# Optimization experiments

Hardware: AMD Instinct MI355X
Metric: run time of the kernel (lower is better)

The kernel has to match this reference:

```python
import jax, jax.numpy as jnp
import numpy as np

B, CI, HW, K, C, NH, L = 512, 3, 28, 28 // 28 and 0 or 7, 1024, 16, 12
K = 7


def setup_inputs() -> dict:
    key = jax.random.key(0)
    ks = jax.random.split(key, 8)
    s = 0.02
    return {
        "x": jax.random.normal(ks[0], (B, CI, HW, HW), jnp.float32),
        "conv_w": jax.random.normal(ks[1], (C, CI, K, K), jnp.float32) * s,  # Conv2d weight [Co,Ci,k,k], shared with deconv
        "ln1_w": jnp.ones((L, C), jnp.float32),
        "ln1_b": jnp.zeros((L, C), jnp.float32),
        "wq": jax.random.normal(ks[2], (L, C, C), jnp.float32) * s,
        "wk": jax.random.normal(ks[3], (L, C, C), jnp.float32) * s,
        "wv": jax.random.normal(ks[4], (L, C, C), jnp.float32) * s,
        "ln2_w": jnp.ones((L, C), jnp.float32),
        "ln2_b": jnp.zeros((L, C), jnp.float32),
        "mlp_w": jax.random.normal(ks[5], (L, C, C), jnp.float32) * s,
        "mlp_b": jnp.zeros((L, C), jnp.float32),
        "out_w": jax.random.normal(ks[6], (C, C), jnp.float32) * s,
        "out_b": jnp.zeros((C,), jnp.float32),
        "head_num": NH,
    }


def _layernorm(x, w, b, eps=1e-5):
    m = jnp.mean(x, axis=-1, keepdims=True)
    v = jnp.var(x, axis=-1, keepdims=True)  # biased var, matches torch LayerNorm
    return (x - m) * jax.lax.rsqrt(v + eps) * w + b


def _attn(h, wq, wk, wv, nh):
    b, t, c = h.shape
    hd = c // nh
    q = (h @ wq.T).reshape(b, t, nh, hd).transpose(0, 2, 1, 3)  # [B,H,T,hd]
    k = (h @ wk.T).reshape(b, t, nh, hd).transpose(0, 2, 1, 3)
    v = (h @ wv.T).reshape(b, t, nh, hd).transpose(0, 2, 1, 3)
    scores = jnp.einsum("bhqd,bhkd->bhqk", q, k) / jnp.sqrt(jnp.float32(hd))
    mask = jnp.tril(jnp.ones((t, t), bool))
    scores = jnp.where(mask, scores, -jnp.inf)
    a = jax.nn.softmax(scores, axis=-1)
    o = jnp.einsum("bhqk,bhkd->bhqd", a, v)
    return o.transpose(0, 2, 1, 3).reshape(b, t, c)


def _forward(x, conv_w, ln1_w, ln1_b, wq, wk, wv, ln2_w, ln2_b, mlp_w, mlp_b, out_w, out_b, head_num):
    b, ci, hh, ww = x.shape
    co, _, k, _ = conv_w.shape
    # thumbnail: bilinear downsample to (k,k) (align_corners=False == half-pixel), then k-strided conv -> [B,Co]
    thumb = jax.image.resize(x, (b, ci, k, k), method="bilinear", antialias=False)
    thumb_tok = jnp.einsum("bcpq,dcpq->bd", thumb, conv_w)
    # kernel==stride conv == patchify + matmul
    hp, wp = hh // k, ww // k
    xp = x.reshape(b, ci, hp, k, wp, k)
    patches = jnp.einsum("bcipjq,dcpq->bdij", xp, conv_w).reshape(b, co, hp * wp)
    h = jnp.concatenate([thumb_tok[:, :, None], patches], axis=-1).transpose(0, 2, 1)  # [B,T=1+hp*wp,C]
    nlayers = ln1_w.shape[0]
    for l in range(nlayers):
        a = _attn(_layernorm(h, ln1_w[l], ln1_b[l]), wq[l], wk[l], wv[l], head_num)
        h = h + a
        m = _layernorm(h, ln2_w[l], ln2_b[l]) @ mlp_w[l].T + mlp_b[l]
        h = h + m
    logits = h @ out_w.T + out_b  # [B,T,C]
    # decode: ConvTranspose2d(kernel=stride=k) with shared weight; input [B,Co,1,T] -> [B,Ci,k,T*k]
    z = logits.transpose(0, 2, 1)  # [B,Co,T]
    t = z.shape[-1]
    out = jnp.einsum("bcs,cdhw->bdhsw", z, conv_w).reshape(b, ci, k, t * k)
    return out


def reference(x, conv_w, ln1_w, ln1_b, wq, wk, wv, ln2_w, ln2_b, mlp_w, mlp_b, out_w, out_b, head_num):
    return _forward(x, conv_w, ln1_w, ln1_b, wq, wk, wv, ln2_w, ln2_b, mlp_w, mlp_b, out_w, out_b, head_num)
```

## Files before the change

### kernel.cpp

```cpp
#include <hip/hip_runtime.h>


typedef unsigned short u16;
typedef short bfrag8 __attribute__((ext_vector_type(8)));
typedef float facc4 __attribute__((ext_vector_type(4)));

__device__ __forceinline__ u16 f2bf(float f) {
  union { float f; unsigned u; } x; x.f = f;
  unsigned r = x.u + 0x7fffu + ((x.u >> 16) & 1u);
  return (u16)(r >> 16);
}
__device__ __forceinline__ float bf2f(u16 h) {
  union { unsigned u; float f; } x; x.u = ((unsigned)h) << 16;
  return x.f;
}

template <int MODE>
__global__ __launch_bounds__(256) void gemm_bt(
    const u16* __restrict__ A, int lda,
    const u16* __restrict__ B0, const u16* __restrict__ B1, const u16* __restrict__ B2,
    int ldb, int K,
    void* __restrict__ outp, long long zstride, int ldo,
    const float* __restrict__ bias)
{
  __shared__ __align__(16) u16 As[128 * 32];
  __shared__ __align__(16) u16 Bs[128 * 32];

  const int m0 = blockIdx.x * 128;
  const int n0 = blockIdx.y * 128;
  const int z  = blockIdx.z;
  const u16* __restrict__ B = (z == 0) ? B0 : ((z == 1) ? B1 : B2);

  const int tid  = threadIdx.x;
  const int wave = tid >> 6;
  const int lane = tid & 63;
  const int wm   = (wave >> 1) * 64;
  const int wn   = (wave & 1) * 64;
  const int lrow = lane & 15;
  const int lquad = lane >> 4;

  facc4 acc[4][4] = {};

  const int c0 = tid;        const int r0 = c0 >> 2; const int k0c = (c0 & 3) << 3;
  const int c1 = tid + 256;  const int r1 = c1 >> 2; const int k1c = (c1 & 3) << 3;

  for (int k0 = 0; k0 < K; k0 += 32) {
    const u16* ga0 = A + (long long)(m0 + r0) * lda + (k0 + k0c);
    const u16* ga1 = A + (long long)(m0 + r1) * lda + (k0 + k1c);
    const u16* gb0 = B + (long long)(n0 + r0) * ldb + (k0 + k0c);
    const u16* gb1 = B + (long long)(n0 + r1) * ldb + (k0 + k1c);
    __builtin_amdgcn_global_load_lds((const __attribute__((address_space(1))) void*)ga0,
                                     (__attribute__((address_space(3))) void*)(As + c0 * 8), 16, 0, 0);
    __builtin_amdgcn_global_load_lds((const __attribute__((address_space(1))) void*)ga1,
                                     (__attribute__((address_space(3))) void*)(As + c1 * 8), 16, 0, 0);
    __builtin_amdgcn_global_load_lds((const __attribute__((address_space(1))) void*)gb0,
                                     (__attribute__((address_space(3))) void*)(Bs + c0 * 8), 16, 0, 0);
    __builtin_amdgcn_global_load_lds((const __attribute__((address_space(1))) void*)gb1,
                                     (__attribute__((address_space(3))) void*)(Bs + c1 * 8), 16, 0, 0);
    __syncthreads();

    bfrag8 af[4], bfr[4];
#pragma unroll
    for (int im = 0; im < 4; ++im)
      af[im] = *(const bfrag8*)(As + (wm + im * 16 + lrow) * 32 + lquad * 8);
#pragma unroll
    for (int in = 0; in < 4; ++in)
      bfr[in] = *(const bfrag8*)(Bs + (wn + in * 16 + lrow) * 32 + lquad * 8);
#pragma unroll
    for (int im = 0; im < 4; ++im)
#pragma unroll
      for (int in = 0; in < 4; ++in)
        acc[im][in] = __builtin_amdgcn_mfma_f32_16x16x32_bf16(af[im], bfr[in], acc[im][in], 0, 0, 0);
    __syncthreads();
  }

#pragma unroll
  for (int in = 0; in < 4; ++in) {
    const int col = n0 + wn + in * 16 + lrow;
    const float bb = bias ? bias[col] : 0.0f;
#pragma unroll
    for (int im = 0; im < 4; ++im) {
#pragma unroll
      for (int r = 0; r < 4; ++r) {
        const int row = m0 + wm + im * 16 + lquad * 4 + r;
        const long long off = (long long)row * ldo + col;
        const float v = acc[im][in][r] + bb;
        if (MODE == 0)       ((float*)outp)[off] = v;
        else if (MODE == 1)  (((u16*)outp) + zstride * z)[off] = f2bf(v);
        else                 ((float*)outp)[off] += v;
      }
    }
  }
}

__global__ __launch_bounds__(256) void ln_kernel(
    const float* __restrict__ h, const float* __restrict__ w,
    const float* __restrict__ b, u16* __restrict__ out)
{
  const long long row = blockIdx.x;
  const float* __restrict__ x = h + row * 1024;
  const int t = threadIdx.x;
  float v0 = x[t], v1 = x[t + 256], v2 = x[t + 512], v3 = x[t + 768];
  float s = v0 + v1 + v2 + v3;
  float q = v0 * v0 + v1 * v1 + v2 * v2 + v3 * v3;
  for (int o = 32; o > 0; o >>= 1) { s += __shfl_down(s, o); q += __shfl_down(q, o); }
  __shared__ float ss[4], sq[4];
  const int wave = t >> 6, lane = t & 63;
  if (lane == 0) { ss[wave] = s; sq[wave] = q; }
  __syncthreads();
  const float st = ss[0] + ss[1] + ss[2] + ss[3];
  const float qt = sq[0] + sq[1] + sq[2] + sq[3];
  const float mean = st * (1.0f / 1024.0f);
  const float var = qt * (1.0f / 1024.0f) - mean * mean;
  const float inv = rsqrtf(var + 1e-5f);
  u16* o2 = out + row * 1024;
  o2[t]       = f2bf((v0 - mean) * inv * w[t]       + b[t]);
  o2[t + 256] = f2bf((v1 - mean) * inv * w[t + 256] + b[t + 256]);
  o2[t + 512] = f2bf((v2 - mean) * inv * w[t + 512] + b[t + 512]);
  o2[t + 768] = f2bf((v3 - mean) * inv * w[t + 768] + b[t + 768]);
}

__global__ __launch_bounds__(256) void attn_kernel(const u16* __restrict__ QKV,
                                                   float* __restrict__ h)
{
  const int blk = blockIdx.x;
  const int b = blk >> 4, head = blk & 15;
  __shared__ float qs[17][64], ks[17][64], vs[17][64];
  __shared__ float sc[17][20];
  const long long base = (long long)b * 17 * 1024 + head * 64;
  const u16* Q  = QKV;
  const u16* Kp = QKV + 8912896LL;
  const u16* V  = QKV + 17825792LL;

  for (int i = threadIdx.x; i < 17 * 64; i += 256) {
    const int t = i >> 6, d = i & 63;
    const long long off = base + (long long)t * 1024 + d;
    qs[t][d] = bf2f(Q[off]); ks[t][d] = bf2f(Kp[off]); vs[t][d] = bf2f(V[off]);
  }
  __syncthreads();

  for (int i = threadIdx.x; i < 289; i += 256) {
    const int tq = i / 17, tk = i % 17;
    float a = 0.0f;
    if (tk <= tq) {
#pragma unroll
      for (int d = 0; d < 64; ++d) a += qs[tq][d] * ks[tk][d];
      a *= 0.125f;
    }
    sc[tq][tk] = a;
  }
  __syncthreads();

  if (threadIdx.x < 17) {
    const int tq = threadIdx.x;
    float m = -1e30f;
    for (int tk = 0; tk <= tq; ++tk) m = fmaxf(m, sc[tq][tk]);
    float s = 0.0f;
    for (int tk = 0; tk <= tq; ++tk) { const float e = __expf(sc[tq][tk] - m); sc[tq][tk] = e; s += e; }
    const float inv = 1.0f / s;
    for (int tk = 0; tk <= tq; ++tk) sc[tq][tk] *= inv;
  }
  __syncthreads();

  for (int i = threadIdx.x; i < 17 * 64; i += 256) {
    const int tq = i >> 6, d = i & 63;
    float a = 0.0f;
    for (int tk = 0; tk <= tq; ++tk) a += sc[tq][tk] * vs[tk][d];
    h[base + (long long)tq * 1024 + d] += a;
  }
}

__global__ void build_p(const float* __restrict__ x, u16* __restrict__ P)
{
  const int n = blockIdx.x;
  const int j = threadIdx.x;
  if (j >= 160) return;
  const int b = n / 17, t = n % 17;
  float val = 0.0f;
  if (j < 147) {
    const int c = j / 49, rem = j % 49, p = rem / 7, q = rem % 7;
    const float* xb = x + (long long)(b * 3 + c) * 784;
    if (t == 0) {
      const int r = 4 * p + 1, cc = 4 * q + 1;
      val = 0.25f * (xb[r * 28 + cc] + xb[r * 28 + cc + 1] +
                     xb[(r + 1) * 28 + cc] + xb[(r + 1) * 28 + cc + 1]);
    } else {
      const int s = t - 1, ii = s >> 2, jj = s & 3;
      val = xb[(7 * ii + p) * 28 + 7 * jj + q];
    }
  }
  P[(long long)n * 160 + j] = f2bf(val);
}

__global__ __launch_bounds__(256) void cvt_conv(const float* __restrict__ cw,
                                                u16* __restrict__ Wc, u16* __restrict__ cw2)
{
  const int i = blockIdx.x * 256 + threadIdx.x;
  if (i < 163840) {
    const int d = i / 160, j = i % 160;
    Wc[i] = (j < 147) ? f2bf(cw[d * 147 + j]) : (u16)0;
  } else {
    const int i2 = i - 163840;
    if (i2 < 262144) {
      const int j = i2 / 1024, c = i2 % 1024;
      cw2[i2] = (j < 147) ? f2bf(cw[c * 147 + j]) : (u16)0;
    }
  }
}

__global__ __launch_bounds__(256) void cvt4(const float* __restrict__ a0, const float* __restrict__ a1,
                                            const float* __restrict__ a2, const float* __restrict__ a3,
                                            u16* __restrict__ o3, u16* __restrict__ om)
{
  const int i = blockIdx.x * 256 + threadIdx.x;
  const int which = i >> 20, off = i & 1048575;
  const float* src = (which == 0) ? a0 : (which == 1) ? a1 : (which == 2) ? a2 : a3;
  const float v = src[off];
  if (which < 3) o3[which * 1048576 + off] = f2bf(v);
  else           om[off] = f2bf(v);
}

__global__ __launch_bounds__(256) void cvtN(const float* __restrict__ in, u16* __restrict__ out, int n)
{
  const int i = blockIdx.x * 256 + threadIdx.x;
  if (i < n) out[i] = f2bf(in[i]);
}

__global__ __launch_bounds__(256) void scatter_out(const float* __restrict__ temp, float* __restrict__ out)
{
  const int i = blockIdx.x * 256 + threadIdx.x;
  if (i >= 1279488) return;
  const int wk = i % 7;
  const int r  = i / 7;
  const int s  = r % 17;
  const int r2 = r / 17;
  const int hk = r2 % 7;
  const int r3 = r2 / 7;
  const int d  = r3 % 3;
  const int b  = r3 / 3;
  out[i] = temp[(long long)(b * 17 + s) * 256 + d * 49 + hk * 7 + wk];
}

extern "C" void kernel_launch(void* const* d_in, const int* in_sizes, int n_in,
                              void* d_out, int out_size, void* d_ws, size_t ws_size,
                              hipStream_t stream)
{
  const float* x     = (const float*)d_in[0];
  const float* convw = (const float*)d_in[1];
  const float* ln1w  = (const float*)d_in[2];
  const float* ln1b  = (const float*)d_in[3];
  const float* wq    = (const float*)d_in[4];
  const float* wk    = (const float*)d_in[5];
  const float* wv    = (const float*)d_in[6];
  const float* ln2w  = (const float*)d_in[7];
  const float* ln2b  = (const float*)d_in[8];
  const float* mlpw  = (const float*)d_in[9];
  const float* mlpb  = (const float*)d_in[10];
  const float* outw  = (const float*)d_in[11];
  const float* outb  = (const float*)d_in[12];

  char* w = (char*)d_ws;
  float* h    = (float*)(w);
  u16*  Abuf  = (u16*)(w + 35651584);
  u16*  QKV   = (u16*)(w + 53477376);
  u16*  wb3   = (u16*)(w + 106954752);
  u16*  wmb   = (u16*)(w + 113246208);
  u16*  Wc    = (u16*)(w + 115343360);
  u16*  cw2   = (u16*)(w + 115671040);
  u16*  P     = (u16*)(w + 116195328);
  if (ws_size < 118980608ULL) return;

  cvt_conv<<<1664, 256, 0, stream>>>(convw, Wc, cw2);
  build_p<<<8704, 192, 0, stream>>>(x, P);
  gemm_bt<0><<<dim3(68, 8, 1), 256, 0, stream>>>(P, 160, Wc, Wc, Wc, 160, 160,
                                                 (void*)h, 0LL, 1024, nullptr);
  for (int l = 0; l < 12; ++l) {
    const size_t wo = (size_t)l * 1048576;
    cvt4<<<16384, 256, 0, stream>>>(wq + wo, wk + wo, wv + wo, mlpw + wo, wb3, wmb);
    ln_kernel<<<8704, 256, 0, stream>>>(h, ln1w + l * 1024, ln1b + l * 1024, Abuf);
    gemm_bt<1><<<dim3(68, 8, 3), 256, 0, stream>>>(Abuf, 1024, wb3, wb3 + 1048576, wb3 + 2097152,
                                                   1024, 1024, (void*)QKV, 8912896LL, 1024, nullptr);
    attn_kernel<<<8192, 256, 0, stream>>>(QKV, h);
    ln_kernel<<<8704, 256, 0, stream>>>(h, ln2w + l * 1024, ln2b + l * 1024, Abuf);
    gemm_bt<2><<<dim3(68, 8, 1), 256, 0, stream>>>(Abuf, 1024, wmb, wmb, wmb,
                                                   1024, 1024, (void*)h, 0LL, 1024, mlpb + l * 1024);
  }
  cvtN<<<34816, 256, 0, stream>>>(h, Abuf, 8912896);
  cvtN<<<4096, 256, 0, stream>>>(outw, wmb, 1048576);
  gemm_bt<1><<<dim3(68, 8, 1), 256, 0, stream>>>(Abuf, 1024, wmb, wmb, wmb,
                                                 1024, 1024, (void*)QKV, 0LL, 1024, outb);
  gemm_bt<0><<<dim3(68, 2, 1), 256, 0, stream>>>(QKV, 1024, cw2, cw2, cw2,
                                                 1024, 1024, (void*)h, 0LL, 256, nullptr);
  scatter_out<<<4998, 256, 0, stream>>>(h, (float*)d_out);
}
```

Before: 3.036 ms.

## Swizzle GEMM LDS layout, coalesce bf16 stores, batch weight conversion, fuse output scatter

Several changes at once. The GEMM's LDS tile now uses an XOR-swizzled layout with hoisted, precomputed addresses to cut bank conflicts. The bf16-output mode stages results through shared memory so global writes are 16-byte coalesced. A new cvt_all kernel converts all layer weights in one launch when the workspace is large, replacing twelve per-layer cvt4 launches. The final scatter_out kernel is dropped, and its index remapping moves into a new GEMM epilogue mode that writes directly to the output. The trade-off is added epilogue syncs and a larger workspace requirement for the batched-conversion path.

```diff
diff --git a/kernel.cpp b/kernel.cpp
--- a/kernel.cpp
+++ b/kernel.cpp
@@ -23,8 +23,9 @@
     void* __restrict__ outp, long long zstride, int ldo,
     const float* __restrict__ bias)
 {
-  __shared__ __align__(16) u16 As[128 * 32];
-  __shared__ __align__(16) u16 Bs[128 * 32];
+  __shared__ __align__(16) u16 smem[8192];
+  u16* const As = smem;
+  u16* const Bs = smem + 4096;
 
   const int m0 = blockIdx.x * 128;
   const int n0 = blockIdx.y * 128;
@@ -41,31 +42,39 @@
 
   facc4 acc[4][4] = {};
 
-  const int c0 = tid;        const int r0 = c0 >> 2; const int k0c = (c0 & 3) << 3;
-  const int c1 = tid + 256;  const int r1 = c1 >> 2; const int k1c = (c1 & 3) << 3;
+  int rA0, g0; { const int rp = tid >> 3, q = tid & 7, qp = q ^ (rp & 3);
+                 rA0 = rp * 2 + (qp >> 2); g0 = qp & 3; }
+  int rA1, g1; { const int s1 = tid + 256, rp = s1 >> 3, q = s1 & 7, qp = q ^ (rp & 3);
+                 rA1 = rp * 2 + (qp >> 2); g1 = qp & 3; }
+  const u16* ga0 = A + (long long)(m0 + rA0) * lda + g0 * 8;
+  const u16* ga1 = A + (long long)(m0 + rA1) * lda + g1 * 8;
+  const u16* gb0 = B + (long long)(n0 + rA0) * ldb + g0 * 8;
+  const u16* gb1 = B + (long long)(n0 + rA1) * ldb + g1 * 8;
+
+  const int ra = wm + lrow;
+  const int pa = (((ra & 1) << 2) | lquad) ^ ((ra >> 1) & 3);
+  const u16* const abase = As + (((ra >> 1) * 8 + pa) << 3);
+  const int rb = wn + lrow;
+  const int pb = (((rb & 1) << 2) | lquad) ^ ((rb >> 1) & 3);
+  const u16* const bbase = Bs + (((rb >> 1) * 8 + pb) << 3);
 
   for (int k0 = 0; k0 < K; k0 += 32) {
-    const u16* ga0 = A + (long long)(m0 + r0) * lda + (k0 + k0c);
-    const u16* ga1 = A + (long long)(m0 + r1) * lda + (k0 + k1c);
-    const u16* gb0 = B + (long long)(n0 + r0) * ldb + (k0 + k0c);
-    const u16* gb1 = B + (long long)(n0 + r1) * ldb + (k0 + k1c);
     __builtin_amdgcn_global_load_lds((const __attribute__((address_space(1))) void*)ga0,
-                                     (__attribute__((address_space(3))) void*)(As + c0 * 8), 16, 0, 0);
+                                     (__attribute__((address_space(3))) void*)(As + tid * 8), 16, 0, 0);
     __builtin_amdgcn_global_load_lds((const __attribute__((address_space(1))) void*)ga1,
-                                     (__attribute__((address_space(3))) void*)(As + c1 * 8), 16, 0, 0);
+                                     (__attribute__((address_space(3))) void*)(As + (tid + 256) * 8), 16, 0, 0);
     __builtin_amdgcn_global_load_lds((const __attribute__((address_space(1))) void*)gb0,
-                                     (__attribute__((address_space(3))) void*)(Bs + c0 * 8), 16, 0, 0);
+                                     (__attribute__((address_space(3))) void*)(Bs + tid * 8), 16, 0, 0);
     __builtin_amdgcn_global_load_lds((const __attribute__((address_space(1))) void*)gb1,
-                                     (__attribute__((address_space(3))) void*)(Bs + c1 * 8), 16, 0, 0);
+                                     (__attribute__((address_space(3))) void*)(Bs + (tid + 256) * 8), 16, 0, 0);
+    ga0 += 32; ga1 += 32; gb0 += 32; gb1 += 32;
     __syncthreads();
 
     bfrag8 af[4], bfr[4];
 #pragma unroll
-    for (int im = 0; im < 4; ++im)
-      af[im] = *(const bfrag8*)(As + (wm + im * 16 + lrow) * 32 + lquad * 8);
-#pragma unroll
-    for (int in = 0; in < 4; ++in)
-      bfr[in] = *(const bfrag8*)(Bs + (wn + in * 16 + lrow) * 32 + lquad * 8);
+    for (int im = 0; im < 4; ++im) af[im] = *(const bfrag8*)(abase + 512 * im);
+#pragma unroll
+    for (int in = 0; in < 4; ++in) bfr[in] = *(const bfrag8*)(bbase + 512 * in);
 #pragma unroll
     for (int im = 0; im < 4; ++im)
 #pragma unroll
@@ -74,20 +83,58 @@
     __syncthreads();
   }
 
+  if (MODE == 1) {
+    u16* const outb = ((u16*)outp) + zstride * z;
+    u16* const Ts = smem;
+#pragma unroll
+    for (int half = 0; half < 2; ++half) {
+      if ((wave >> 1) == half) {
+#pragma unroll
+        for (int in = 0; in < 4; ++in) {
+          const int col = wn + in * 16 + lrow;
+          const float bb = bias ? bias[n0 + col] : 0.0f;
+#pragma unroll
+          for (int im = 0; im < 4; ++im)
+#pragma unroll
+            for (int r = 0; r < 4; ++r)
+              Ts[(im * 16 + lquad * 4 + r) * 128 + col] = f2bf(acc[im][in][r] + bb);
+        }
+      }
+      __syncthreads();
+#pragma unroll
+      for (int it = 0; it < 4; ++it) {
+        const int g = it * 256 + tid;
+        const int row = g >> 4, colg = g & 15;
+        *(uint4*)(outb + (long long)(m0 + half * 64 + row) * ldo + n0 + colg * 8) =
+            *(const uint4*)(Ts + row * 128 + colg * 8);
+      }
+      __syncthreads();
+    }
+    return;
+  }
+
 #pragma unroll
   for (int in = 0; in < 4; ++in) {
     const int col = n0 + wn + in * 16 + lrow;
-    const float bb = bias ? bias[col] : 0.0f;
+    const float bb = (MODE != 3 && bias) ? bias[col] : 0.0f;
 #pragma unroll
     for (int im = 0; im < 4; ++im) {
 #pragma unroll
       for (int r = 0; r < 4; ++r) {
         const int row = m0 + wm + im * 16 + lquad * 4 + r;
-        const long long off = (long long)row * ldo + col;
         const float v = acc[im][in][r] + bb;
-        if (MODE == 0)       ((float*)outp)[off] = v;
-        else if (MODE == 1)  (((u16*)outp) + zstride * z)[off] = f2bf(v);
-        else                 ((float*)outp)[off] += v;
+        if (MODE == 0) {
+          ((float*)outp)[(long long)row * ldo + col] = v;
+        } else if (MODE == 2) {
+          ((float*)outp)[(long long)row * ldo + col] += v;
+        } else {
+          if (col < 147) {
+            const int b = row / 17, s = row - b * 17;
+            const int d = col / 49, rem = col - d * 49;
+            const int hk = rem / 7, wk = rem - hk * 7;
+            ((float*)outp)[(long long)((b * 3 + d) * 7 + hk) * 119 + s * 7 + wk] = v;
+          }
+        }
       }
     }
   }
@@ -208,6 +255,27 @@
   }
 }
 
+__global__ __launch_bounds__(256) void cvt_all(
+    const float* __restrict__ wq, const float* __restrict__ wk,
+    const float* __restrict__ wv, const float* __restrict__ mlpw,
+    const float* __restrict__ outw, u16* __restrict__ wAll)
+{
+  const int i = blockIdx.x * 256 + threadIdx.x;
+  const int which = i >> 18;
+  const int off = i & 262143;
+  const float4* src;
+  if (which < 48) {
+    const int layer = which >> 2, sub = which & 3;
+    const float* base = (sub == 0) ? wq : (sub == 1) ? wk : (sub == 2) ? wv : mlpw;
+    src = (const float4*)(base + (size_t)layer * 1048576) + off;
+  } else {
+    src = (const float4*)outw + off;
+  }
+  const float4 v = *src;
+  ushort4 o; o.x = f2bf(v.x); o.y = f2bf(v.y); o.z = f2bf(v.z); o.w = f2bf(v.w);
+  *(ushort4*)(wAll + (size_t)which * 1048576 + (size_t)off * 4) = o;
+}
+
 __global__ __launch_bounds__(256) void cvt4(const float* __restrict__ a0, const float* __restrict__ a1,
                                             const float* __restrict__ a2, const float* __restrict__ a3,
                                             u16* __restrict__ o3, u16* __restrict__ om)
@@ -224,21 +292,6 @@
 {
   const int i = blockIdx.x * 256 + threadIdx.x;
   if (i < n) out[i] = f2bf(in[i]);
-}
-
-__global__ __launch_bounds__(256) void scatter_out(const float* __restrict__ temp, float* __restrict__ out)
-{
-  const int i = blockIdx.x * 256 + threadIdx.x;
-  if (i >= 1279488) return;
-  const int wk = i % 7;
-  const int r  = i / 7;
-  const int s  = r % 17;
-  const int r2 = r / 17;
-  const int hk = r2 % 7;
-  const int r3 = r2 / 7;
-  const int d  = r3 % 3;
-  const int b  = r3 / 3;
-  out[i] = temp[(long long)(b * 17 + s) * 256 + d * 49 + hk * 7 + wk];
 }
 
 extern "C" void kernel_launch(void* const* d_in, const int* in_sizes, int n_in,
@@ -260,36 +313,69 @@
   const float* outb  = (const float*)d_in[12];
 
   char* w = (char*)d_ws;
-  float* h    = (float*)(w);
-  u16*  Abuf  = (u16*)(w + 35651584);
-  u16*  QKV   = (u16*)(w + 53477376);
-  u16*  wb3   = (u16*)(w + 106954752);
-  u16*  wmb   = (u16*)(w + 113246208);
-  u16*  Wc    = (u16*)(w + 115343360);
-  u16*  cw2   = (u16*)(w + 115671040);
-  u16*  P     = (u16*)(w + 116195328);
-  if (ws_size < 118980608ULL) return;
-
-  cvt_conv<<<1664, 256, 0, stream>>>(convw, Wc, cw2);
-  build_p<<<8704, 192, 0, stream>>>(x, P);
-  gemm_bt<0><<<dim3(68, 8, 1), 256, 0, stream>>>(P, 160, Wc, Wc, Wc, 160, 160,
-                                                 (void*)h, 0LL, 1024, nullptr);
-  for (int l = 0; l < 12; ++l) {
-    const size_t wo = (size_t)l * 1048576;
-    cvt4<<<16384, 256, 0, stream>>>(wq + wo, wk + wo, wv + wo, mlpw + wo, wb3, wmb);
-    ln_kernel<<<8704, 256, 0, stream>>>(h, ln1w + l * 1024, ln1b + l * 1024, Abuf);
-    gemm_bt<1><<<dim3(68, 8, 3), 256, 0, stream>>>(Abuf, 1024, wb3, wb3 + 1048576, wb3 + 2097152,
-                                                   1024, 1024, (void*)QKV, 8912896LL, 1024, nullptr);
-    attn_kernel<<<8192, 256, 0, stream>>>(QKV, h);
-    ln_kernel<<<8704, 256, 0, stream>>>(h, ln2w + l * 1024, ln2b + l * 1024, Abuf);
-    gemm_bt<2><<<dim3(68, 8, 1), 256, 0, stream>>>(Abuf, 1024, wmb, wmb, wmb,
-                                                   1024, 1024, (void*)h, 0LL, 1024, mlpb + l * 1024);
-  }
-  cvtN<<<34816, 256, 0, stream>>>(h, Abuf, 8912896);
-  cvtN<<<4096, 256, 0, stream>>>(outw, wmb, 1048576);
-  gemm_bt<1><<<dim3(68, 8, 1), 256, 0, stream>>>(Abuf, 1024, wmb, wmb, wmb,
-                                                 1024, 1024, (void*)QKV, 0LL, 1024, outb);
-  gemm_bt<0><<<dim3(68, 2, 1), 256, 0, stream>>>(QKV, 1024, cw2, cw2, cw2,
-                                                 1024, 1024, (void*)h, 0LL, 256, nullptr);
-  scatter_out<<<4998, 256, 0, stream>>>(h, (float*)d_out);
-}
+  const bool big = (ws_size >= 213352448ULL);
+
+  if (big) {
+    float* h   = (float*)(w);
+    u16* Abuf  = (u16*)(w + 35651584);
+    u16* QKV   = (u16*)(w + 53477376);
+    u16* wAll  = (u16*)(w + 106954752);
+    u16* Wc    = (u16*)(w + 209715200);
+    u16* cw2   = (u16*)(w + 210042880);
+    u16* P     = (u16*)(w + 210567168);
+
+    cvt_all<<<50176, 256, 0, stream>>>(wq, wk, wv, mlpw, outw, wAll);
+    cvt_conv<<<1664, 256, 0, stream>>>(convw, Wc, cw2);
+    build_p<<<8704, 192, 0, stream>>>(x, P);
+    gemm_bt<0><<<dim3(68, 8, 1), 256, 0, stream>>>(P, 160, Wc, Wc, Wc, 160, 160,
+                                                   (void*)h, 0LL, 1024, nullptr);
+    for (int l = 0; l < 12; ++l) {
+      u16* wl = wAll + (size_t)l * 4194304;
+      ln_kernel<<<8704, 256, 0, stream>>>(h, ln1w + l * 1024, ln1b + l * 1024, Abuf);
+      gemm_bt<1><<<dim3(68, 8, 3), 256, 0, stream>>>(Abuf, 1024, wl, wl + 1048576, wl + 2097152,
+                                                     1024, 1024, (void*)QKV, 8912896LL, 1024, nullptr);
+      attn_kernel<<<8192, 256, 0, stream>>>(QKV, h);
+      ln_kernel<<<8704, 256, 0, stream>>>(h, ln2w + l * 1024, ln2b + l * 1024, Abuf);
+      gemm_bt<2><<<dim3(68, 8, 1), 256, 0, stream>>>(Abuf, 1024, wl + 3145728, wl, wl,
+                                                     1024, 1024, (void*)h, 0LL, 1024, mlpb + l * 1024);
+    }
+    u16* wout = wAll + (size_t)48 * 1048576;
+    cvtN<<<34816, 256, 0, stream>>>(h, Abuf, 8912896);
+    gemm_bt<1><<<dim3(68, 8, 1), 256, 0, stream>>>(Abuf, 1024, wout, wout, wout,
+                                                   1024, 1024, (void*)QKV, 0LL, 1024, outb);
+    gemm_bt<3><<<dim3(68, 2, 1), 256, 0, stream>>>(QKV, 1024, cw2, cw2, cw2,
+                                                   1024, 1024, d_out, 0LL, 0, nullptr);
+  } else {
+    if (ws_size < 118980608ULL) return;
+    float* h   = (float*)(w);
+    u16* Abuf  = (u16*)(w + 35651584);
+    u16* QKV   = (u16*)(w + 53477376);
+    u16* wb3   = (u16*)(w + 106954752);
+    u16* wmb   = (u16*)(w + 113246208);
+    u16* Wc    = (u16*)(w + 115343360);
+    u16* cw2   = (u16*)(w + 115671040);
+    u16* P     = (u16*)(w + 116195328);
+
+    cvt_conv<<<1664, 256, 0, stream>>>(convw, Wc, cw2);
+    build_p<<<8704, 192, 0, stream>>>(x, P);
+    gemm_bt<0><<<dim3(68, 8, 1), 256, 0, stream>>>(P, 160, Wc, Wc, Wc, 160, 160,
+                                                   (void*)h, 0LL, 1024, nullptr);
+    for (int l = 0; l < 12; ++l) {
+      const size_t wo = (size_t)l * 1048576;
+      cvt4<<<16384, 256, 0, stream>>>(wq + wo, wk + wo, wv + wo, mlpw + wo, wb3, wmb);
+      ln_kernel<<<8704, 256, 0, stream>>>(h, ln1w + l * 1024, ln1b + l * 1024, Abuf);
+      gemm_bt<1><<<dim3(68, 8, 3), 256, 0, stream>>>(Abuf, 1024, wb3, wb3 + 1048576, wb3 + 2097152,
+                                                     1024, 1024, (void*)QKV, 8912896LL, 1024, nullptr);
+      attn_kernel<<<8192, 256, 0, stream>>>(QKV, h);
+      ln_kernel<<<8704, 256, 0, stream>>>(h, ln2w + l * 1024, ln2b + l * 1024, Abuf);
+      gemm_bt<2><<<dim3(68, 8, 1), 256, 0, stream>>>(Abuf, 1024, wmb, wmb, wmb,
+                                                     1024, 1024, (void*)h, 0LL, 1024, mlpb + l * 1024);
+    }
+    cvtN<<<34816, 256, 0, stream>>>(h, Abuf, 8912896);
+    cvtN<<<4096, 256, 0, stream>>>(outw, wmb, 1048576);
+    gemm_bt<1><<<dim3(68, 8, 1), 256, 0, stream>>>(Abuf, 1024, wmb, wmb, wmb,
+                                                   1024, 1024, (void*)QKV, 0LL, 1024, outb);
+    gemm_bt<3><<<dim3(68, 2, 1), 256, 0, stream>>>(QKV, 1024, cw2, cw2, cw2,
+                                                   1024, 1024, d_out, 0LL, 0, nullptr);
+  }
+}
```

Result: no change. 3.052 ms (+0.5%).
